# Performance work log

Measured on AMD Instinct MI355X. Metric: run time of the kernel, lower is better.

Reference implementation:

```python
import jax, jax.numpy as jnp
import numpy as np

N_HEAD = 16
D_LATENT = 64
N_EMBD = 1024
D_HEAD = N_EMBD // N_HEAD          # 64
D_HEAD_E = D_HEAD // 2             # 32 (rotary part)
D_HEAD_C = D_HEAD // 2             # 32 (content part)
BLOCK_SIZE = 1024


def rope_cache(dim, max_seq_len, theta=10000.0):
    inv_freq = 1.0 / (theta ** (jnp.arange(0, dim, 2, dtype=jnp.float32) / dim))
    t = jnp.arange(max_seq_len, dtype=jnp.float32)
    freqs = t[:, None] * inv_freq[None, :]            # [T, dim/2]
    emb = jnp.concatenate([freqs, freqs], axis=-1)    # [T, dim]
    return jnp.cos(emb), jnp.sin(emb)


def apply_rope(x, cos, sin):
    # x: [B, H, T, C]; interleaved rotate-half as in the torch module
    B, H, T, C = x.shape
    xf = x.astype(jnp.float32)
    xr = xf.reshape(B, H, T, C // 2, 2)
    x1, x2 = xr[..., 0], xr[..., 1]
    rotated = jnp.stack([-x2, x1], axis=-1).reshape(B, H, T, C)
    c = cos[:T][None, None]  # [1,1,T,C]
    s = sin[:T][None, None]
    return (xf * c + rotated * s).astype(x.dtype)


def setup_inputs() -> dict:
    key = jax.random.key(0)
    ks = jax.random.split(key, 10)
    std = 0.02
    inp = {
        "x": jax.random.normal(ks[0], (4, 1024, N_EMBD), dtype=jnp.float32),
        "Wq_down": jax.random.normal(ks[1], (N_EMBD, N_HEAD * D_LATENT), dtype=jnp.float32) * std,
        "Wk_down": jax.random.normal(ks[2], (N_EMBD, N_HEAD * D_LATENT), dtype=jnp.float32) * std,
        "Wv_down": jax.random.normal(ks[3], (N_EMBD, N_HEAD * D_LATENT), dtype=jnp.float32) * std,
        "Wq_up_c": jax.random.normal(ks[4], (D_LATENT, D_HEAD_C), dtype=jnp.float32) * std,
        "Wq_up_e": jax.random.normal(ks[5], (D_LATENT, D_HEAD_E), dtype=jnp.float32) * std,
        "Wk_up_c": jax.random.normal(ks[6], (D_LATENT, D_HEAD_C), dtype=jnp.float32) * std,
        "Wk_up_e": jax.random.normal(ks[7], (D_LATENT, D_HEAD_E), dtype=jnp.float32) * std,
        "Wv_up": jax.random.normal(ks[8], (D_LATENT, D_HEAD), dtype=jnp.float32) * std,
        "Wc": jax.random.normal(ks[9], (N_EMBD, N_EMBD), dtype=jnp.float32) * std,
    }
    return inp


def reference(x, Wq_down, Wk_down, Wv_down, Wq_up_c, Wq_up_e, Wk_up_c, Wk_up_e, Wv_up, Wc):
    B, T, C = x.shape
    # MLA down projections -> per-head latents [B, T, H, d_latent]
    q_lat = jnp.einsum('btc,cd->btd', x, Wq_down).reshape(B, T, N_HEAD, D_LATENT)
    k_lat = jnp.einsum('btc,cd->btd', x, Wk_down).reshape(B, T, N_HEAD, D_LATENT)
    v_lat = jnp.einsum('btc,cd->btd', x, Wv_down).reshape(B, T, N_HEAD, D_LATENT)
    # Up projections, fused with the transpose(1,2): [B, H, T, d]
    q_c = jnp.einsum('bthl,ld->bhtd', q_lat, Wq_up_c)
    q_e = jnp.einsum('bthl,ld->bhtd', q_lat, Wq_up_e)
    k_c = jnp.einsum('bthl,ld->bhtd', k_lat, Wk_up_c)
    k_e = jnp.einsum('bthl,ld->bhtd', k_lat, Wk_up_e)
    v = jnp.einsum('bthl,ld->bhtd', v_lat, Wv_up)
    # Partial RoPE on the 'e' halves
    cos, sin = rope_cache(D_HEAD_E, BLOCK_SIZE)
    q = jnp.concatenate([q_c, apply_rope(q_e, cos, sin)], axis=-1)  # [B,H,T,d_head]
    k = jnp.concatenate([k_c, apply_rope(k_e, cos, sin)], axis=-1)
    # Causal scaled dot-product attention (== SDPA is_causal=True, no dropout)
    scale = 1.0 / jnp.sqrt(jnp.array(q.shape[-1], dtype=jnp.float32))
    att = jnp.einsum('bhqd,bhkd->bhqk', q, k) * scale
    causal = jnp.tril(jnp.ones((T, T), dtype=bool))
    att = jnp.where(causal[None, None], att, jnp.float32(-1e30))
    att = jax.nn.softmax(att, axis=-1)
    y = jnp.einsum('bhqk,bhkd->bhqd', att, v)
    y = y.transpose(0, 2, 1, 3).reshape(B, T, C)
    y = jnp.einsum('btc,cd->btd', y, Wc)
    return y, k_lat, v_lat
```

## Files before the change

### kernel.cpp

```cpp
#include <hip/hip_runtime.h>

typedef unsigned short u16;
typedef unsigned int   u32;
typedef __bf16 bf16x8 __attribute__((ext_vector_type(8)));
typedef float  f32x4  __attribute__((ext_vector_type(4)));


__device__ __forceinline__ float b2f(u16 u) {
    u32 x = ((u32)u) << 16; float f; __builtin_memcpy(&f, &x, 4); return f;
}
__device__ __forceinline__ u16 f2b(float f) {
    u32 x; __builtin_memcpy(&x, &f, 4);
    u32 r = x + 0x7FFFu + ((x >> 16) & 1u);
    return (u16)(r >> 16);
}

#define GLD_LDS16(src, dst) \
  __builtin_amdgcn_global_load_lds((const __attribute__((address_space(1))) unsigned int*)(src), \
                                   (__attribute__((address_space(3))) unsigned int*)(dst), 16, 0, 0)

__global__ __launch_bounds__(256) void prep(
    const float* __restrict__ x, u16* __restrict__ xb,
    const float* __restrict__ W0, const float* __restrict__ W1,
    const float* __restrict__ W2, const float* __restrict__ W3,
    u16* __restrict__ T0, u16* __restrict__ T1,
    u16* __restrict__ T2, u16* __restrict__ T3)
{
    const int bx = blockIdx.x, tid = threadIdx.x;
    if (bx >= 1024) {
        int i0 = ((bx - 1024) * 256 + tid) * 8;
        #pragma unroll
        for (int j = 0; j < 8; j++) xb[i0 + j] = f2b(x[i0 + j]);
        return;
    }
    __shared__ u16 t[64][65];
    int z = bx >> 8, xy = bx & 255;
    const float* W = (z == 0) ? W0 : (z == 1) ? W1 : (z == 2) ? W2 : W3;
    u16* O = (z == 0) ? T0 : (z == 1) ? T1 : (z == 2) ? T2 : T3;
    int r0 = (xy >> 4) * 64, c0 = (xy & 15) * 64;
    int row = tid >> 2, seg = (tid & 3) * 16;
    #pragma unroll
    for (int i = 0; i < 16; i++)
        t[row][seg + i] = f2b(W[(size_t)(r0 + row) * 1024 + c0 + seg + i]);
    __syncthreads();
    #pragma unroll
    for (int i = 0; i < 16; i++)
        O[(size_t)(c0 + row) * 1024 + r0 + seg + i] = t[seg + i][row];
}

#define PIPE_GEMM_LOOP(A_, Bt_)                                                 \
    const int skq0 = w, skq1 = w + 4;                                           \
    const int srow0 = skq0 * 16 + (l >> 2), srow1 = skq1 * 16 + (l >> 2);       \
    const int skoff0 = (((l & 3) ^ ((srow0 ^ (srow0 >> 2)) & 3)) * 8);          \
    const int skoff1 = (((l & 3) ^ ((srow1 ^ (srow1 >> 2)) & 3)) * 8);          \
    f32x4 acc[4][4] = {};                                                       \
    {                                                                           \
        const int k0 = 0;                                                       \
        GLD_LDS16(A_  + (size_t)(m0 + srow0) * K + k0 + skoff0, sA0 + skq0 * 1024); \
        GLD_LDS16(A_  + (size_t)(m0 + srow1) * K + k0 + skoff1, sA0 + skq1 * 1024); \
        GLD_LDS16(Bt_ + (size_t)(n0 + srow0) * K + k0 + skoff0, sB0 + skq0 * 1024); \
        GLD_LDS16(Bt_ + (size_t)(n0 + srow1) * K + k0 + skoff1, sB0 + skq1 * 1024); \
    }                                                                           \
    for (int kt = 0; kt < 32; ++kt) {                                           \
        char* cA = (kt & 1) ? sA1 : sA0;                                        \
        char* cB = (kt & 1) ? sB1 : sB0;                                        \
        if (kt < 31) {                                                          \
            char* nA = (kt & 1) ? sA0 : sA1;                                    \
            char* nB = (kt & 1) ? sB0 : sB1;                                    \
            const int k0 = (kt + 1) * 32;                                       \
            GLD_LDS16(A_  + (size_t)(m0 + srow0) * K + k0 + skoff0, nA + skq0 * 1024); \
            GLD_LDS16(A_  + (size_t)(m0 + srow1) * K + k0 + skoff1, nA + skq1 * 1024); \
            GLD_LDS16(Bt_ + (size_t)(n0 + srow0) * K + k0 + skoff0, nB + skq0 * 1024); \
            GLD_LDS16(Bt_ + (size_t)(n0 + srow1) * K + k0 + skoff1, nB + skq1 * 1024); \
            asm volatile("s_waitcnt vmcnt(4)" ::: "memory");                    \
        } else {                                                                \
            asm volatile("s_waitcnt vmcnt(0)" ::: "memory");                    \
        }                                                                       \
        __builtin_amdgcn_s_barrier();                                           \
        __builtin_amdgcn_sched_barrier(0);                                      \
        bf16x8 af[4], bf[4];                                                    \
        _Pragma("unroll")                                                       \
        for (int mi = 0; mi < 4; ++mi) {                                        \
            int row = wr * 64 + mi * 16 + fr;                                   \
            int off = row * 64 + ((fg ^ ((row ^ (row >> 2)) & 3)) << 4);        \
            af[mi] = *(const bf16x8*)(cA + off);                                \
        }                                                                       \
        _Pragma("unroll")                                                       \
        for (int ni = 0; ni < 4; ++ni) {                                        \
            int row = wc * 64 + ni * 16 + fr;                                   \
            int off = row * 64 + ((fg ^ ((row ^ (row >> 2)) & 3)) << 4);        \
            bf[ni] = *(const bf16x8*)(cB + off);                                \
        }                                                                       \
        _Pragma("unroll")                                                       \
        for (int mi = 0; mi < 4; ++mi)                                          \
            _Pragma("unroll")                                                   \
            for (int ni = 0; ni < 4; ++ni)                                      \
                acc[mi][ni] = __builtin_amdgcn_mfma_f32_16x16x32_bf16(          \
                    af[mi], bf[ni], acc[mi][ni], 0, 0, 0);                      \
        __builtin_amdgcn_sched_barrier(0);                                      \
        __builtin_amdgcn_s_barrier();                                           \
        __builtin_amdgcn_sched_barrier(0);                                      \
    }

__global__ __launch_bounds__(256) void gemm_fused(
    const u16* __restrict__ A,
    const u16* __restrict__ Bt0, const u16* __restrict__ Bt1, const u16* __restrict__ Bt2,
    const float* __restrict__ Wqc, const float* __restrict__ Wqe,
    const float* __restrict__ Wkc, const float* __restrict__ Wke,
    const float* __restrict__ Wv,
    float* __restrict__ klat_out, float* __restrict__ vlat_out,
    u16* __restrict__ Qo, u16* __restrict__ Ko, u16* __restrict__ Vto)
{
    constexpr int K = 1024, N = 1024;
    __shared__ __align__(16) char smem[40960];
    char* sA0 = smem;
    char* sA1 = smem + 8192;
    char* sB0 = smem + 16384;
    char* sB1 = smem + 24576;
    u16 (*sW)[64][8] = (u16(*)[64][8])(smem + 32768);
    const int tid = threadIdx.x;
    const int w = tid >> 6, l = tid & 63;
    const int z = blockIdx.z;
    const u16* Bt = (z == 0) ? Bt0 : (z == 1) ? Bt1 : Bt2;
    const int m0 = blockIdx.x * 128, n0 = blockIdx.y * 128;
    const int wr = w >> 1, wc = w & 1;
    const int fr = l & 15, fg = l >> 4;

    for (int e = tid; e < 4096; e += 256) {
        int k = e >> 6, n = e & 63;
        float v;
        if (z == 2)      v = Wv[k * 64 + n];
        else if (z == 0) v = (n < 32) ? Wqc[k * 32 + n] : Wqe[k * 32 + n - 32];
        else             v = (n < 32) ? Wkc[k * 32 + n] : Wke[k * 32 + n - 32];
        sW[k >> 3][n][k & 7] = f2b(v);
    }

    PIPE_GEMM_LOOP(A, Bt)

    if (z) {
        float* L = (z == 1) ? klat_out : vlat_out;
        #pragma unroll
        for (int mi = 0; mi < 4; ++mi)
            #pragma unroll
            for (int ni = 0; ni < 4; ++ni)
                #pragma unroll
                for (int rr = 0; rr < 4; ++rr) {
                    int r = m0 + wr * 64 + mi * 16 + fg * 4 + rr;
                    int c = n0 + wc * 64 + ni * 16 + fr;
                    L[(size_t)r * N + c] = acc[mi][ni][rr];
                }
    }

    __syncthreads();

    char* sL = smem + w * 8192;
    #pragma unroll
    for (int mi = 0; mi < 4; ++mi)
        #pragma unroll
        for (int ni = 0; ni < 4; ++ni)
            #pragma unroll
            for (int rr = 0; rr < 4; ++rr) {
                int row = mi * 16 + fg * 4 + rr;
                int lat = ni * 16 + fr;
                int byte = row * 128 + ((((lat >> 3) ^ (row & 7)) << 4) | ((lat & 7) << 1));
                *(u16*)(sL + byte) = f2b(acc[mi][ni][rr]);
            }
    __syncthreads();

    bf16x8 af2[4][2], bf2[4][2];
    #pragma unroll
    for (int mi = 0; mi < 4; ++mi)
        #pragma unroll
        for (int kk = 0; kk < 2; ++kk) {
            int row = mi * 16 + fr;
            af2[mi][kk] = *(const bf16x8*)(sL + row * 128 + (((kk * 4 + fg) ^ (row & 7)) << 4));
        }
    #pragma unroll
    for (int ni = 0; ni < 4; ++ni)
        #pragma unroll
        for (int kk = 0; kk < 2; ++kk)
            bf2[ni][kk] = *(const bf16x8*)&sW[kk * 4 + fg][ni * 16 + fr][0];

    f32x4 o2[4][4] = {};
    #pragma unroll
    for (int kk = 0; kk < 2; ++kk)
        #pragma unroll
        for (int mi = 0; mi < 4; ++mi)
            #pragma unroll
            for (int ni = 0; ni < 4; ++ni)
                o2[mi][ni] = __builtin_amdgcn_mfma_f32_16x16x32_bf16(af2[mi][kk], bf2[ni][kk], o2[mi][ni], 0, 0, 0);

    const int rbase = m0 + wr * 64;
    const int b = rbase >> 10, tbase = rbase & 1023;
    const int h = blockIdx.y * 2 + wc;
    const size_t obase = ((size_t)(b * 16 + h)) << 16;

    if (z == 2) {
        #pragma unroll
        for (int mi = 0; mi < 4; ++mi)
            #pragma unroll
            for (int ni = 0; ni < 4; ++ni) {
                union { u16 u[4]; uint2 v; } pk;
                #pragma unroll
                for (int rr = 0; rr < 4; ++rr) pk.u[rr] = f2b(o2[mi][ni][rr]);
                int t0 = tbase + mi * 16 + fg * 4;
                int d = ni * 16 + fr;
                *(uint2*)(Vto + obase + (size_t)d * 1024 + t0) = pk.v;
            }
    } else {
        const float qscale = (z == 0) ? 0.125f : 1.0f;
        const float rf = __expf(-(float)fr * 0.5756462732485115f);
        u16* O = (z == 0) ? Qo : Ko;
        #pragma unroll
        for (int mi = 0; mi < 4; ++mi) {
            #pragma unroll
            for (int rr = 0; rr < 4; ++rr) {
                int t = tbase + mi * 16 + fg * 4 + rr;
                float ang = (float)t * rf;
                float sn = __sinf(ang), cs = __cosf(ang);
                #pragma unroll
                for (int ni = 0; ni < 4; ++ni) {
                    float a = o2[mi][ni][rr];
                    float p = __shfl_xor(a, 1);
                    if (ni >= 2)
                        a = a * cs + ((fr & 1) ? p : -p) * sn;
                    a *= qscale;
                    O[obase + (size_t)t * 64 + ni * 16 + fr] = f2b(a);
                }
            }
        }
    }
}

__global__ __launch_bounds__(256) void gemm128_out(
    const u16* __restrict__ A, const u16* __restrict__ Bt, float* __restrict__ Cf)
{
    constexpr int K = 1024, N = 1024;
    __shared__ __align__(16) char smem[32768];
    char* sA0 = smem;
    char* sA1 = smem + 8192;
    char* sB0 = smem + 16384;
    char* sB1 = smem + 24576;
    const int tid = threadIdx.x;
    const int w = tid >> 6, l = tid & 63;
    const int m0 = blockIdx.x * 128, n0 = blockIdx.y * 128;
    const int wr = w >> 1, wc = w & 1;
    const int fr = l & 15, fg = l >> 4;

    PIPE_GEMM_LOOP(A, Bt)

    #pragma unroll
    for (int mi = 0; mi < 4; ++mi)
        #pragma unroll
        for (int ni = 0; ni < 4; ++ni)
            #pragma unroll
            for (int rr = 0; rr < 4; ++rr) {
                int r = m0 + wr * 64 + mi * 16 + fg * 4 + rr;
                int c = n0 + wc * 64 + ni * 16 + fr;
                Cf[(size_t)r * N + c] = acc[mi][ni][rr];
            }
}

__global__ __launch_bounds__(256) void attn(
    const u16* __restrict__ Q, const u16* __restrict__ K,
    const u16* __restrict__ Vt, u16* __restrict__ Y)
{
    __shared__ __align__(16) char sK[2][8192];
    __shared__ __align__(16) char sV[2][8192];
    __shared__ __align__(16) char sP[4][2048];
    const int tid = threadIdx.x, w = tid >> 6, l = tid & 63;
    const int bh = blockIdx.x, p = blockIdx.y;
    const int qtA = p, qtB = 15 - p;
    const int fr = l & 15, fg = l >> 4;
    const size_t base = (size_t)bh << 16;
    const int b = bh >> 4, h = bh & 15;

    const int skb = (((l & 7) * 16) ^ ((l >> 3) << 4)) >> 1;
    const int srow = l >> 3;

    bf16x8 qfA[2], qfB[2];
    #pragma unroll
    for (int kk = 0; kk < 2; kk++) {
        qfA[kk] = *(const bf16x8*)(Q + base + (size_t)(qtA * 64 + w * 16 + fr) * 64 + kk * 32 + fg * 8);
        qfB[kk] = *(const bf16x8*)(Q + base + (size_t)(qtB * 64 + w * 16 + fr) * 64 + kk * 32 + fg * 8);
    }

    f32x4 oA[4] = {}, oB[4] = {};
    float mA[4], lsA[4] = {0.f, 0.f, 0.f, 0.f};
    float mB[4], lsB[4] = {0.f, 0.f, 0.f, 0.f};
    #pragma unroll
    for (int rr = 0; rr < 4; rr++) { mA[rr] = -30000.0f; mB[rr] = -30000.0f; }

    auto stage = [&](int buf, int kv0) {
        #pragma unroll
        for (int ci = 0; ci < 2; ++ci) {
            int c = w + ci * 4;
            int row = c * 8 + srow;
            GLD_LDS16(K  + base + (size_t)(kv0 + row) * 64 + skb, sK[buf] + c * 1024);
            GLD_LDS16(Vt + base + (size_t)row * 1024 + kv0 + skb, sV[buf] + c * 1024);
        }
    };

    auto tile_step = [&](int buf, int kv0, int qt, bool diag,
                         bf16x8 (&qf)[2], f32x4 (&o)[4], float (&m)[4], float (&ls)[4]) {
        f32x4 s[4] = {};
        #pragma unroll
        for (int kk = 0; kk < 2; kk++)
            #pragma unroll
            for (int ni = 0; ni < 4; ni++) {
                int off = (ni * 16 + fr) * 128 + ((kk * 64 + fg * 16) ^ ((fr & 7) << 4));
                bf16x8 kf = *(const bf16x8*)(sK[buf] + off);
                s[ni] = __builtin_amdgcn_mfma_f32_16x16x32_bf16(qf[kk], kf, s[ni], 0, 0, 0);
            }
        if (diag) {
            int q0w = qt * 64 + w * 16;
            #pragma unroll
            for (int ni = 0; ni < 4; ni++) {
                int kj = kv0 + ni * 16 + fr;
                #pragma unroll
                for (int rr = 0; rr < 4; rr++) {
                    int qi = q0w + fg * 4 + rr;
                    if (kj > qi) s[ni][rr] = -30000.0f;
                }
            }
        }
        float alpha[4];
        #pragma unroll
        for (int rr = 0; rr < 4; rr++) {
            float mx = fmaxf(fmaxf(s[0][rr], s[1][rr]), fmaxf(s[2][rr], s[3][rr]));
            mx = fmaxf(mx, __shfl_xor(mx, 1));
            mx = fmaxf(mx, __shfl_xor(mx, 2));
            mx = fmaxf(mx, __shfl_xor(mx, 4));
            mx = fmaxf(mx, __shfl_xor(mx, 8));
            float mn = fmaxf(m[rr], mx);
            alpha[rr] = __expf(m[rr] - mn);
            m[rr] = mn;
        }
        float psum[4] = {0.f, 0.f, 0.f, 0.f};
        #pragma unroll
        for (int ni = 0; ni < 4; ni++)
            #pragma unroll
            for (int rr = 0; rr < 4; rr++) {
                float pv = __expf(s[ni][rr] - m[rr]);
                s[ni][rr] = pv;
                psum[rr] += pv;
            }
        #pragma unroll
        for (int rr = 0; rr < 4; rr++) ls[rr] = ls[rr] * alpha[rr] + psum[rr];
        #pragma unroll
        for (int ni = 0; ni < 4; ni++)
            #pragma unroll
            for (int rr = 0; rr < 4; rr++) o[ni][rr] *= alpha[rr];
        #pragma unroll
        for (int ni = 0; ni < 4; ni++)
            #pragma unroll
            for (int rr = 0; rr < 4; rr++) {
                int prow = fg * 4 + rr, col = ni * 16 + fr;
                *(u16*)(sP[w] + prow * 128 + ((col * 2) ^ ((prow & 7) << 4))) = f2b(s[ni][rr]);
            }
        #pragma unroll
        for (int kk = 0; kk < 2; kk++) {
            int poff = fr * 128 + ((kk * 64 + fg * 16) ^ ((fr & 7) << 4));
            bf16x8 pa = *(const bf16x8*)(sP[w] + poff);
            #pragma unroll
            for (int ni = 0; ni < 4; ni++) {
                int voff = (ni * 16 + fr) * 128 + ((kk * 64 + fg * 16) ^ ((fr & 7) << 4));
                bf16x8 vf = *(const bf16x8*)(sV[buf] + voff);
                o[ni] = __builtin_amdgcn_mfma_f32_16x16x32_bf16(pa, vf, o[ni], 0, 0, 0);
            }
        }
    };

    stage(0, 0);
    asm volatile("s_waitcnt vmcnt(0)" ::: "memory");
    __syncthreads();
    int cur = 0;
    for (int kt = 0; kt <= qtB; ++kt) {
        if (kt < qtB) stage(cur ^ 1, (kt + 1) * 64);
        if (kt <= qtA) tile_step(cur, kt * 64, qtA, kt == qtA, qfA, oA, mA, lsA);
        tile_step(cur, kt * 64, qtB, kt == qtB, qfB, oB, mB, lsB);
        asm volatile("s_waitcnt vmcnt(0)" ::: "memory");
        __syncthreads();
        cur ^= 1;
    }

    #pragma unroll
    for (int rr = 0; rr < 4; rr++) {
        float tA = lsA[rr], tB = lsB[rr];
        #pragma unroll
        for (int sft = 1; sft < 16; sft <<= 1) {
            tA += __shfl_xor(tA, sft);
            tB += __shfl_xor(tB, sft);
        }
        lsA[rr] = 1.0f / tA;
        lsB[rr] = 1.0f / tB;
    }
    #pragma unroll
    for (int ni = 0; ni < 4; ni++)
        #pragma unroll
        for (int rr = 0; rr < 4; rr++) {
            int qiA = qtA * 64 + w * 16 + fg * 4 + rr;
            int qiB = qtB * 64 + w * 16 + fg * 4 + rr;
            int d = h * 64 + ni * 16 + fr;
            Y[((size_t)(b * 1024 + qiA)) * 1024 + d] = f2b(oA[ni][rr] * lsA[rr]);
            Y[((size_t)(b * 1024 + qiB)) * 1024 + d] = f2b(oB[ni][rr] * lsB[rr]);
        }
}

extern "C" void kernel_launch(void* const* d_in, const int* in_sizes, int n_in,
                              void* d_out, int out_size, void* d_ws, size_t ws_size,
                              hipStream_t stream) {
    const float* x    = (const float*)d_in[0];
    const float* Wqd  = (const float*)d_in[1];
    const float* Wkd  = (const float*)d_in[2];
    const float* Wvd  = (const float*)d_in[3];
    const float* Wqc  = (const float*)d_in[4];
    const float* Wqe  = (const float*)d_in[5];
    const float* Wkc  = (const float*)d_in[6];
    const float* Wke  = (const float*)d_in[7];
    const float* Wvu  = (const float*)d_in[8];
    const float* Wc   = (const float*)d_in[9];

    float* dout     = (float*)d_out;
    float* y_out    = dout;
    float* klat_out = dout + 4194304;
    float* vlat_out = dout + 8388608;

    const size_t MiB = 1024 * 1024;
    char* ws = (char*)d_ws;
    u16* WqdT = (u16*)(ws);
    u16* WkdT = (u16*)(ws + 2  * MiB);
    u16* WvdT = (u16*)(ws + 4  * MiB);
    u16* WcT  = (u16*)(ws + 6  * MiB);
    u16* xb   = (u16*)(ws + 8  * MiB);
    u16* Qw   = (u16*)(ws + 16 * MiB);
    u16* Kw   = (u16*)(ws + 24 * MiB);
    u16* Vtw  = (u16*)(ws + 32 * MiB);
    u16* Ya   = (u16*)(ws + 40 * MiB);

    prep<<<dim3(3072), 256, 0, stream>>>(x, xb, Wqd, Wkd, Wvd, Wc,
                                         WqdT, WkdT, WvdT, WcT);
    gemm_fused<<<dim3(32, 8, 3), 256, 0, stream>>>(xb, WqdT, WkdT, WvdT,
                                                   Wqc, Wqe, Wkc, Wke, Wvu,
                                                   klat_out, vlat_out,
                                                   Qw, Kw, Vtw);
    attn<<<dim3(64, 8), 256, 0, stream>>>(Qw, Kw, Vtw, Ya);
    gemm128_out<<<dim3(32, 8), 256, 0, stream>>>(Ya, WcT, y_out);
}
```

Before: 107.7 us.

## Replace double-buffered GEMM loop with single-buffer BK64; split attention tiles per block

```diff
diff --git a/kernel.cpp b/kernel.cpp
--- a/kernel.cpp
+++ b/kernel.cpp
@@ -48,58 +48,44 @@
         O[(size_t)(c0 + row) * 1024 + r0 + seg + i] = t[seg + i][row];
 }
 
-#define PIPE_GEMM_LOOP(A_, Bt_)                                                 \
-    const int skq0 = w, skq1 = w + 4;                                           \
-    const int srow0 = skq0 * 16 + (l >> 2), srow1 = skq1 * 16 + (l >> 2);       \
-    const int skoff0 = (((l & 3) ^ ((srow0 ^ (srow0 >> 2)) & 3)) * 8);          \
-    const int skoff1 = (((l & 3) ^ ((srow1 ^ (srow1 >> 2)) & 3)) * 8);          \
-    f32x4 acc[4][4] = {};                                                       \
-    {                                                                           \
-        const int k0 = 0;                                                       \
-        GLD_LDS16(A_  + (size_t)(m0 + srow0) * K + k0 + skoff0, sA0 + skq0 * 1024); \
-        GLD_LDS16(A_  + (size_t)(m0 + srow1) * K + k0 + skoff1, sA0 + skq1 * 1024); \
-        GLD_LDS16(Bt_ + (size_t)(n0 + srow0) * K + k0 + skoff0, sB0 + skq0 * 1024); \
-        GLD_LDS16(Bt_ + (size_t)(n0 + srow1) * K + k0 + skoff1, sB0 + skq1 * 1024); \
-    }                                                                           \
-    for (int kt = 0; kt < 32; ++kt) {                                           \
-        char* cA = (kt & 1) ? sA1 : sA0;                                        \
-        char* cB = (kt & 1) ? sB1 : sB0;                                        \
-        if (kt < 31) {                                                          \
-            char* nA = (kt & 1) ? sA0 : sA1;                                    \
-            char* nB = (kt & 1) ? sB0 : sB1;                                    \
-            const int k0 = (kt + 1) * 32;                                       \
-            GLD_LDS16(A_  + (size_t)(m0 + srow0) * K + k0 + skoff0, nA + skq0 * 1024); \
-            GLD_LDS16(A_  + (size_t)(m0 + srow1) * K + k0 + skoff1, nA + skq1 * 1024); \
-            GLD_LDS16(Bt_ + (size_t)(n0 + srow0) * K + k0 + skoff0, nB + skq0 * 1024); \
-            GLD_LDS16(Bt_ + (size_t)(n0 + srow1) * K + k0 + skoff1, nB + skq1 * 1024); \
-            asm volatile("s_waitcnt vmcnt(4)" ::: "memory");                    \
-        } else {                                                                \
-            asm volatile("s_waitcnt vmcnt(0)" ::: "memory");                    \
-        }                                                                       \
-        __builtin_amdgcn_s_barrier();                                           \
-        __builtin_amdgcn_sched_barrier(0);                                      \
-        bf16x8 af[4], bf[4];                                                    \
-        _Pragma("unroll")                                                       \
-        for (int mi = 0; mi < 4; ++mi) {                                        \
-            int row = wr * 64 + mi * 16 + fr;                                   \
-            int off = row * 64 + ((fg ^ ((row ^ (row >> 2)) & 3)) << 4);        \
-            af[mi] = *(const bf16x8*)(cA + off);                                \
-        }                                                                       \
-        _Pragma("unroll")                                                       \
-        for (int ni = 0; ni < 4; ++ni) {                                        \
-            int row = wc * 64 + ni * 16 + fr;                                   \
-            int off = row * 64 + ((fg ^ ((row ^ (row >> 2)) & 3)) << 4);        \
-            bf[ni] = *(const bf16x8*)(cB + off);                                \
-        }                                                                       \
-        _Pragma("unroll")                                                       \
-        for (int mi = 0; mi < 4; ++mi)                                          \
-            _Pragma("unroll")                                                   \
-            for (int ni = 0; ni < 4; ++ni)                                      \
-                acc[mi][ni] = __builtin_amdgcn_mfma_f32_16x16x32_bf16(          \
-                    af[mi], bf[ni], acc[mi][ni], 0, 0, 0);                      \
-        __builtin_amdgcn_sched_barrier(0);                                      \
-        __builtin_amdgcn_s_barrier();                                           \
-        __builtin_amdgcn_sched_barrier(0);                                      \
+#define M97_GEMM_LOOP(A_, Bt_)                                                 \
+    const int skb = (((l & 7) * 16) ^ ((l >> 3) << 4)) >> 1;                   \
+    const int srow = l >> 3;                                                   \
+    f32x4 acc[4][4] = {};                                                      \
+    for (int kt = 0; kt < 16; ++kt) {                                          \
+        const int k0 = kt * 64;                                                \
+        if (kt > 0) __syncthreads();                                           \
+        _Pragma("unroll")                                                      \
+        for (int ci = 0; ci < 4; ++ci) {                                       \
+            int c = w + ci * 4;                                                \
+            int row = c * 8 + srow;                                            \
+            GLD_LDS16(A_  + (size_t)(m0 + row) * K + k0 + skb, sA + c * 1024); \
+            GLD_LDS16(Bt_ + (size_t)(n0 + row) * K + k0 + skb, sB + c * 1024); \
+        }                                                                      \
+        asm volatile("s_waitcnt vmcnt(0)" ::: "memory");                       \
+        __syncthreads();                                                       \
+        _Pragma("unroll")                                                      \
+        for (int kk = 0; kk < 2; ++kk) {                                       \
+            bf16x8 af[4], bf[4];                                               \
+            _Pragma("unroll")                                                  \
+            for (int mi = 0; mi < 4; ++mi) {                                   \
+                int row = wr * 64 + mi * 16 + fr;                              \
+                int off = row * 128 + ((kk * 64 + fg * 16) ^ ((fr & 7) << 4)); \
+                af[mi] = *(const bf16x8*)(sA + off);                           \
+            }                                                                  \
+            _Pragma("unroll")                                                  \
+            for (int ni = 0; ni < 4; ++ni) {                                   \
+                int row = wc * 64 + ni * 16 + fr;                              \
+                int off = row * 128 + ((kk * 64 + fg * 16) ^ ((fr & 7) << 4)); \
+                bf[ni] = *(const bf16x8*)(sB + off);                           \
+            }                                                                  \
+            _Pragma("unroll")                                                  \
+            for (int mi = 0; mi < 4; ++mi)                                     \
+                _Pragma("unroll")                                              \
+                for (int ni = 0; ni < 4; ++ni)                                 \
+                    acc[mi][ni] = __builtin_amdgcn_mfma_f32_16x16x32_bf16(     \
+                        af[mi], bf[ni], acc[mi][ni], 0, 0, 0);                 \
+        }                                                                      \
     }
 
 __global__ __launch_bounds__(256) void gemm_fused(
@@ -113,10 +99,8 @@
 {
     constexpr int K = 1024, N = 1024;
     __shared__ __align__(16) char smem[40960];
-    char* sA0 = smem;
-    char* sA1 = smem + 8192;
-    char* sB0 = smem + 16384;
-    char* sB1 = smem + 24576;
+    char* sA = smem;
+    char* sB = smem + 16384;
     u16 (*sW)[64][8] = (u16(*)[64][8])(smem + 32768);
     const int tid = threadIdx.x;
     const int w = tid >> 6, l = tid & 63;
@@ -135,7 +119,7 @@
         sW[k >> 3][n][k & 7] = f2b(v);
     }
 
-    PIPE_GEMM_LOOP(A, Bt)
+    M97_GEMM_LOOP(A, Bt)
 
     if (z) {
         float* L = (z == 1) ? klat_out : vlat_out;
@@ -236,18 +220,15 @@
     const u16* __restrict__ A, const u16* __restrict__ Bt, float* __restrict__ Cf)
 {
     constexpr int K = 1024, N = 1024;
-    __shared__ __align__(16) char smem[32768];
-    char* sA0 = smem;
-    char* sA1 = smem + 8192;
-    char* sB0 = smem + 16384;
-    char* sB1 = smem + 24576;
+    __shared__ __align__(16) char sA[16384];
+    __shared__ __align__(16) char sB[16384];
     const int tid = threadIdx.x;
     const int w = tid >> 6, l = tid & 63;
     const int m0 = blockIdx.x * 128, n0 = blockIdx.y * 128;
     const int wr = w >> 1, wc = w & 1;
     const int fr = l & 15, fg = l >> 4;
 
-    PIPE_GEMM_LOOP(A, Bt)
+    M97_GEMM_LOOP(A, Bt)
 
     #pragma unroll
     for (int mi = 0; mi < 4; ++mi)
@@ -269,27 +250,25 @@
     __shared__ __align__(16) char sV[2][8192];
     __shared__ __align__(16) char sP[4][2048];
     const int tid = threadIdx.x, w = tid >> 6, l = tid & 63;
-    const int bh = blockIdx.x, p = blockIdx.y;
-    const int qtA = p, qtB = 15 - p;
+    const int bh = blockIdx.x;
+    const int qt = 15 - blockIdx.y;
     const int fr = l & 15, fg = l >> 4;
     const size_t base = (size_t)bh << 16;
     const int b = bh >> 4, h = bh & 15;
+    const int q0w = qt * 64 + w * 16;
 
     const int skb = (((l & 7) * 16) ^ ((l >> 3) << 4)) >> 1;
     const int srow = l >> 3;
 
-    bf16x8 qfA[2], qfB[2];
-    #pragma unroll
-    for (int kk = 0; kk < 2; kk++) {
-        qfA[kk] = *(const bf16x8*)(Q + base + (size_t)(qtA * 64 + w * 16 + fr) * 64 + kk * 32 + fg * 8);
-        qfB[kk] = *(const bf16x8*)(Q + base + (size_t)(qtB * 64 + w * 16 + fr) * 64 + kk * 32 + fg * 8);
-    }
-
-    f32x4 oA[4] = {}, oB[4] = {};
-    float mA[4], lsA[4] = {0.f, 0.f, 0.f, 0.f};
-    float mB[4], lsB[4] = {0.f, 0.f, 0.f, 0.f};
-    #pragma unroll
-    for (int rr = 0; rr < 4; rr++) { mA[rr] = -30000.0f; mB[rr] = -30000.0f; }
+    bf16x8 qf[2];
+    #pragma unroll
+    for (int kk = 0; kk < 2; kk++)
+        qf[kk] = *(const bf16x8*)(Q + base + (size_t)(q0w + fr) * 64 + kk * 32 + fg * 8);
+
+    f32x4 o[4] = {};
+    float m[4], ls[4] = {0.f, 0.f, 0.f, 0.f};
+    #pragma unroll
+    for (int rr = 0; rr < 4; rr++) m[rr] = -30000.0f;
 
     auto stage = [&](int buf, int kv0) {
         #pragma unroll
@@ -301,19 +280,24 @@
         }
     };
 
-    auto tile_step = [&](int buf, int kv0, int qt, bool diag,
-                         bf16x8 (&qf)[2], f32x4 (&o)[4], float (&m)[4], float (&ls)[4]) {
+    stage(0, 0);
+    asm volatile("s_waitcnt vmcnt(0)" ::: "memory");
+    __syncthreads();
+    int cur = 0;
+    for (int kt = 0; kt <= qt; ++kt) {
+        const int kv0 = kt * 64;
+        if (kt < qt) stage(cur ^ 1, kv0 + 64);
+
         f32x4 s[4] = {};
         #pragma unroll
         for (int kk = 0; kk < 2; kk++)
             #pragma unroll
             for (int ni = 0; ni < 4; ni++) {
                 int off = (ni * 16 + fr) * 128 + ((kk * 64 + fg * 16) ^ ((fr & 7) << 4));
-                bf16x8 kf = *(const bf16x8*)(sK[buf] + off);
+                bf16x8 kf = *(const bf16x8*)(sK[cur] + off);
                 s[ni] = __builtin_amdgcn_mfma_f32_16x16x32_bf16(qf[kk], kf, s[ni], 0, 0, 0);
             }
-        if (diag) {
-            int q0w = qt * 64 + w * 16;
+        if (kt == qt) {
             #pragma unroll
             for (int ni = 0; ni < 4; ni++) {
                 int kj = kv0 + ni * 16 + fr;
@@ -365,20 +349,10 @@
             #pragma unroll
             for (int ni = 0; ni < 4; ni++) {
                 int voff = (ni * 16 + fr) * 128 + ((kk * 64 + fg * 16) ^ ((fr & 7) << 4));
-                bf16x8 vf = *(const bf16x8*)(sV[buf] + voff);
+                bf16x8 vf = *(const bf16x8*)(sV[cur] + voff);
                 o[ni] = __builtin_amdgcn_mfma_f32_16x16x32_bf16(pa, vf, o[ni], 0, 0, 0);
             }
         }
-    };
-
-    stage(0, 0);
-    asm volatile("s_waitcnt vmcnt(0)" ::: "memory");
-    __syncthreads();
-    int cur = 0;
-    for (int kt = 0; kt <= qtB; ++kt) {
-        if (kt < qtB) stage(cur ^ 1, (kt + 1) * 64);
-        if (kt <= qtA) tile_step(cur, kt * 64, qtA, kt == qtA, qfA, oA, mA, lsA);
-        tile_step(cur, kt * 64, qtB, kt == qtB, qfB, oB, mB, lsB);
         asm volatile("s_waitcnt vmcnt(0)" ::: "memory");
         __syncthreads();
         cur ^= 1;
@@ -386,24 +360,20 @@
 
     #pragma unroll
     for (int rr = 0; rr < 4; rr++) {
-        float tA = lsA[rr], tB = lsB[rr];
-        #pragma unroll
-        for (int sft = 1; sft < 16; sft <<= 1) {
-            tA += __shfl_xor(tA, sft);
-            tB += __shfl_xor(tB, sft);
-        }
-        lsA[rr] = 1.0f / tA;
-        lsB[rr] = 1.0f / tB;
+        float tot = ls[rr];
+        tot += __shfl_xor(tot, 1);
+        tot += __shfl_xor(tot, 2);
+        tot += __shfl_xor(tot, 4);
+        tot += __shfl_xor(tot, 8);
+        ls[rr] = 1.0f / tot;
     }
     #pragma unroll
     for (int ni = 0; ni < 4; ni++)
         #pragma unroll
         for (int rr = 0; rr < 4; rr++) {
-            int qiA = qtA * 64 + w * 16 + fg * 4 + rr;
-            int qiB = qtB * 64 + w * 16 + fg * 4 + rr;
-            int d = h * 64 + ni * 16 + fr;
-            Y[((size_t)(b * 1024 + qiA)) * 1024 + d] = f2b(oA[ni][rr] * lsA[rr]);
-            Y[((size_t)(b * 1024 + qiB)) * 1024 + d] = f2b(oB[ni][rr] * lsB[rr]);
+            int qi = q0w + fg * 4 + rr;
+            size_t yoff = ((size_t)(b * 1024 + qi)) * 1024 + h * 64 + ni * 16 + fr;
+            Y[yoff] = f2b(o[ni][rr] * ls[rr]);
         }
 }
 
@@ -444,6 +414,6 @@
                                                    Wqc, Wqe, Wkc, Wke, Wvu,
                                                    klat_out, vlat_out,
                                                    Qw, Kw, Vtw);
-    attn<<<dim3(64, 8), 256, 0, stream>>>(Qw, Kw, Vtw, Ya);
+    attn<<<dim3(64, 16), 256, 0, stream>>>(Qw, Kw, Vtw, Ya);
     gemm128_out<<<dim3(32, 8), 256, 0, stream>>>(Ya, WcT, y_out);
 }
```

After: 98.33 us. 8.7% less time.
